# Optimization experiments

Hardware: AMD Instinct MI355X
Metric: run time of the kernel (lower is better)

## Reference

```python
import jax, jax.numpy as jnp
import numpy as np

B, K, D = 8192, 8192, 512

def setup_inputs() -> dict:
    key = jax.random.key(0)
    k1, k2 = jax.random.split(key)
    z_e = jax.random.normal(k1, (B, D), dtype=jnp.float32)
    # codebook: kaiming-uniform-initialized parameter; random normal scaled similarly is fine for a numeric baseline
    codebook = jax.random.normal(k2, (K, D), dtype=jnp.float32)
    return {"z_e": z_e, "codebook": codebook}

def reference(z_e, codebook):
    # Euclidean distances via dot-product expansion (same math as
    # torch.norm(z_e[:,None]-codebook[None], dim=-1) without the [B,K,D] intermediate):
    # d^2 = ||z||^2 - 2 z.c + ||c||^2
    z_sq = jnp.sum(z_e * z_e, axis=-1, keepdims=True)          # [B,1]
    c_sq = jnp.sum(codebook * codebook, axis=-1)               # [K]
    cross = jnp.einsum('bd,kd->bk', z_e, codebook)             # [B,K] GEMM
    d2 = jnp.maximum(z_sq - 2.0 * cross + c_sq[None, :], 0.0)  # clamp fp negatives
    distances = jnp.sqrt(d2)                                   # [B,K]
    indices = jnp.argmin(distances, axis=-1)                   # [B]
    z_q = jnp.take(codebook, indices, axis=0)                  # [B,D] gather
    return (z_q, indices)
```

## Files before the change

kernel.cpp:

```cpp
#include <hip/hip_runtime.h>


constexpr int Bn = 8192;
constexpr int Kn = 8192;
constexpr int Dn = 512;

using half8  = __attribute__((ext_vector_type(8)))  _Float16;
using f32x16 = __attribute__((ext_vector_type(16))) float;

#define WS_CSQ  0u
#define WS_ZSQ  (32u*1024u)
#define WS_MAX  (64u*1024u)
#define WS_CNT  (64u*1024u + 64u)
#define WS_WL   (96u*1024u)
#define WS_PART (1u*1024u*1024u)
#define WS_P2   WS_PART
#define WS_CIMG (10u*1024u*1024u)
#define WS_ZIMG (19u*1024u*1024u)

typedef __attribute__((address_space(3))) void       as3_void;
typedef const __attribute__((address_space(1))) void as1_cvoid;

#define MFMA16 __builtin_amdgcn_mfma_f32_32x32x16_f16


__global__ __launch_bounds__(256) void prep_kernel(const float* __restrict__ Z,
                                                   const float* __restrict__ Cb,
                                                   char* __restrict__ ws) {
  const int w = threadIdx.x >> 6, lane = threadIdx.x & 63;
  const int rid = blockIdx.x * 4 + w;
  if (blockIdx.x == 0 && threadIdx.x == 0) *(int*)(ws + WS_CNT) = 0;
  const bool isZ = rid < Bn;
  const int r = isZ ? rid : rid - Bn;
  const float* src = (isZ ? Z : Cb) + (size_t)r * Dn + lane * 8;
  const float4 v0 = *reinterpret_cast<const float4*>(src);
  const float4 v1 = *reinterpret_cast<const float4*>(src + 4);
  const float f[8] = {v0.x, v0.y, v0.z, v0.w, v1.x, v1.y, v1.z, v1.w};
  float ss = 0.f;
  _Float16 h[8];
#pragma unroll
  for (int j = 0; j < 8; ++j) { ss += f[j] * f[j]; h[j] = (_Float16)f[j]; }
#pragma unroll
  for (int off = 32; off; off >>= 1) ss += __shfl_xor(ss, off);
  const half8 vh = {h[0], h[1], h[2], h[3], h[4], h[5], h[6], h[7]};
  const int kt = lane >> 1, kh = lane & 1;
  int grp, rr, tbase, fr;
  char* img;
  if (isZ) {
    grp = (r >> 5) & 7; rr = r & 31; tbase = (r >> 8) * 33; fr = 512;
    img = ws + WS_ZIMG;
  } else {
    grp = (r >> 5) & 3; rr = r & 31; tbase = (r >> 7) * 33; fr = 256;
    img = ws + WS_CIMG;
  }
  const size_t chunk = (size_t)(tbase + kt) * fr + grp * 64 + kh * 32 + rr;
  *reinterpret_cast<half8*>(img + chunk * 16) = vh;
  if (lane < 2) {
    half8 ev = {0, 0, 0, 0, 0, 0, 0, 0};
    if (lane == 0) {
      if (isZ) { ev[0] = (_Float16)1.f; ev[1] = (_Float16)1.f; }
      else {
        const _Float16 hi = (_Float16)(-0.5f * ss);
        ev[0] = hi; ev[1] = (_Float16)(-0.5f * ss - (float)hi);
      }
    }
    const size_t ec = (size_t)(tbase + 32) * fr + grp * 64 + lane * 32 + rr;
    *reinterpret_cast<half8*>(img + ec * 16) = ev;
  }
  if (lane == 0) {
    if (isZ) ((float*)(ws + WS_ZSQ))[r] = ss;
    else {
      ((float*)(ws + WS_CSQ))[r] = ss;
      atomicMax((int*)(ws + WS_MAX), __float_as_int(ss));
    }
  }
}

__global__ __launch_bounds__(256, 2) void vq_pass1(char* __restrict__ ws) {
  __shared__ uint4 lds4[1536];
  char* lds = (char*)lds4;
  const int t = threadIdx.x, lane = t & 63, w = t >> 6;
  const int wm = w >> 1, wn = w & 1;
  const int zblk = blockIdx.x >> 4, split = blockIdx.x & 15;
  const int r31 = lane & 31, kh = lane >> 5;
  const char* CI = ws + WS_CIMG;
  const char* ZI = ws + WS_ZIMG;
  const size_t l16 = (size_t)lane * 16;
  const size_t zsrc = (size_t)zblk * 33 * 8192 + (size_t)w * 2048 + l16;
  const size_t abase = (size_t)(wm * 2) * 1024 + l16;

  float qs1[4], qs2[4];
  int qi1[4];
#pragma unroll
  for (int nb = 0; nb < 4; ++nb) { qs1[nb] = -3e38f; qs2[nb] = -3e38f; qi1[nb] = 0x7fffffff; }

  f32x16 acc[2][4] = {};
  half8 aA0, aA1, aB0, aB1;

  auto STAGE = [&](int kv, int bsel) {
    const char* s = ZI + zsrc + (size_t)kv * 8192;
    char* d = lds + bsel * 8192 + w * 2048;
    __builtin_amdgcn_global_load_lds((as1_cvoid*)(s), (as3_void*)(d), 16, 0, 0);
    __builtin_amdgcn_global_load_lds((as1_cvoid*)(s + 1024), (as3_void*)(d + 1024), 16, 0, 0);
  };

  STAGE(0, 0);
  STAGE(1, 1);
  {
    const char* s = CI + (size_t)(split * 4 * 33 + 0) * 4096 + abase;
    aA0 = *reinterpret_cast<const half8*>(s);
    aA1 = *reinterpret_cast<const half8*>(s + 1024);
  }
  asm volatile("s_waitcnt vmcnt(0)" ::: "memory");
  __builtin_amdgcn_s_barrier();

  int kt = 0, panel = 0, cur = 0, stg = 2;
#pragma unroll 2
  for (int u = 0; u < 132; ++u) {
    int k1 = kt + 1, p1 = panel;
    if (k1 == 33) { k1 = 0; ++p1; }
    int k2 = kt + 2, p2v = panel;
    if (k2 >= 33) { k2 -= 33; ++p2v; }
    if (u + 1 < 132) {
      const char* s = CI + (size_t)((split * 4 + p1) * 33 + k1) * 4096 + abase;
      if ((u & 1) == 0) {
        aB0 = *reinterpret_cast<const half8*>(s);
        aB1 = *reinterpret_cast<const half8*>(s + 1024);
      } else {
        aA0 = *reinterpret_cast<const half8*>(s);
        aA1 = *reinterpret_cast<const half8*>(s + 1024);
      }
    }
    if (u + 2 < 132) STAGE(k2, stg);
    const char* bb = lds + cur * 8192 + (size_t)wn * 4096 + l16;
    const half8 b0 = *reinterpret_cast<const half8*>(bb);
    const half8 b1 = *reinterpret_cast<const half8*>(bb + 1024);
    const half8 b2 = *reinterpret_cast<const half8*>(bb + 2048);
    const half8 b3 = *reinterpret_cast<const half8*>(bb + 3072);
    const half8 a0 = (u & 1) ? aB0 : aA0;
    const half8 a1 = (u & 1) ? aB1 : aA1;
    acc[0][0] = MFMA16(a0, b0, acc[0][0], 0, 0, 0);
    acc[0][1] = MFMA16(a0, b1, acc[0][1], 0, 0, 0);
    acc[0][2] = MFMA16(a0, b2, acc[0][2], 0, 0, 0);
    acc[0][3] = MFMA16(a0, b3, acc[0][3], 0, 0, 0);
    acc[1][0] = MFMA16(a1, b0, acc[1][0], 0, 0, 0);
    acc[1][1] = MFMA16(a1, b1, acc[1][1], 0, 0, 0);
    acc[1][2] = MFMA16(a1, b2, acc[1][2], 0, 0, 0);
    acc[1][3] = MFMA16(a1, b3, acc[1][3], 0, 0, 0);
    if (kt == 32) {
      const int cbase = split * 512 + panel * 128 + wm * 64 + 4 * kh;
#pragma unroll
      for (int nb = 0; nb < 4; ++nb) {
        float m1 = qs1[nb], m2 = qs2[nb];
        int i1 = qi1[nb];
#pragma unroll
        for (int ms = 0; ms < 2; ++ms)
#pragma unroll
          for (int r = 0; r < 16; ++r) {
            const float a = acc[ms][nb][r];
            const int ci = cbase + ms * 32 + (r & 3) + 8 * (r >> 2);
            const bool gt = (a > m1) || (a == m1 && ci < i1);
            const float nm2 = gt ? m1 : fmaxf(m2, a);
            m1 = gt ? a : m1;
            i1 = gt ? ci : i1;
            m2 = nm2;
          }
        qs1[nb] = m1; qs2[nb] = m2; qi1[nb] = i1;
      }
#pragma unroll
      for (int ms = 0; ms < 2; ++ms)
#pragma unroll
        for (int nb = 0; nb < 4; ++nb) acc[ms][nb] = (f32x16)0.f;
    }
    if (u < 130) asm volatile("s_waitcnt vmcnt(4)" ::: "memory");
    else         asm volatile("s_waitcnt vmcnt(2)" ::: "memory");
    __builtin_amdgcn_s_barrier();
    ++kt;
    if (kt == 33) { kt = 0; ++panel; }
    cur = (cur == 2) ? 0 : cur + 1;
    stg = (stg == 2) ? 0 : stg + 1;
  }

  float4* part = (float4*)(ws + WS_PART);
  const int bucket = split * 4 + wm * 2 + kh;
#pragma unroll
  for (int nb = 0; nb < 4; ++nb) {
    const int row = zblk * 256 + wn * 128 + nb * 32 + r31;
    part[(size_t)row * 64 + bucket] =
        make_float4(-2.f * qs1[nb], (float)qi1[nb], -2.f * qs2[nb], 0.f);
  }
}

__global__ __launch_bounds__(64) void gather_finalize(const float* __restrict__ Z,
                                                      const float* __restrict__ Cb,
                                                      char* __restrict__ ws,
                                                      float* __restrict__ zq,
                                                      float* __restrict__ idx_out) {
  const int row = blockIdx.x, l = threadIdx.x;
  const float4 q = ((const float4*)(ws + WS_PART))[(size_t)row * 64 + l];
  float s1 = q.x;
  int i1 = (int)q.y;
#pragma unroll
  for (int off = 1; off <= 32; off <<= 1) {
    const float os = __shfl_xor(s1, off); const int oi = __shfl_xor(i1, off);
    if (os < s1 || (os == s1 && oi < i1)) { s1 = os; i1 = oi; }
  }
  const float zs = ((const float*)(ws + WS_ZSQ))[row];
  const float cmax = __int_as_float(*(const int*)(ws + WS_MAX));
  const float thr = s1 + 4.0e-3f * sqrtf(zs * cmax) + 0.05f;
  int cnt = (q.x <= thr ? 1 : 0) + (q.z <= thr ? 1 : 0);
  int hide = (q.z <= thr) ? 1 : 0;
#pragma unroll
  for (int off = 1; off <= 32; off <<= 1) {
    cnt += __shfl_xor(cnt, off);
    hide |= __shfl_xor(hide, off);
  }
  if (cnt >= 5 || hide) {
    if (l == 0) {
      const int pos = atomicAdd((int*)(ws + WS_CNT), 1);
      if (pos < Bn) ((int*)(ws + WS_WL))[pos] = row;
    }
    return;
  }
  const float* csq = (const float*)(ws + WS_CSQ);
  const float4 z0 = *reinterpret_cast<const float4*>(Z + (size_t)row * Dn + l * 8);
  const float4 z1 = *reinterpret_cast<const float4*>(Z + (size_t)row * Dn + l * 8 + 4);
  float mycand = (q.x <= thr) ? q.x : 3e38f;
  const int myid = (int)q.y;
  float best_s = 3e38f;
  int best_i = 0x7fffffff;
  for (int it = 0; it < 4; ++it) {
    float cs_ = mycand;
    int ci_ = myid;
#pragma unroll
    for (int off = 1; off <= 32; off <<= 1) {
      const float os = __shfl_xor(cs_, off); const int oi = __shfl_xor(ci_, off);
      if (os < cs_ || (os == cs_ && oi < ci_)) { cs_ = os; ci_ = oi; }
    }
    if (cs_ > thr) break;
    if (myid == ci_) mycand = 3e38f;
    const float4 c0 = *reinterpret_cast<const float4*>(Cb + (size_t)ci_ * Dn + l * 8);
    const float4 c1 = *reinterpret_cast<const float4*>(Cb + (size_t)ci_ * Dn + l * 8 + 4);
    float pa = z0.x * c0.x + z0.y * c0.y + z0.z * c0.z + z0.w * c0.w +
               z1.x * c1.x + z1.y * c1.y + z1.z * c1.z + z1.w * c1.w;
#pragma unroll
    for (int off = 1; off <= 32; off <<= 1) pa += __shfl_xor(pa, off);
    const float se = csq[ci_] - 2.f * pa;
    if (se < best_s || (se == best_s && ci_ < best_i)) { best_s = se; best_i = ci_; }
  }
  const float4 o0 = *reinterpret_cast<const float4*>(Cb + (size_t)best_i * Dn + l * 8);
  const float4 o1 = *reinterpret_cast<const float4*>(Cb + (size_t)best_i * Dn + l * 8 + 4);
  *reinterpret_cast<float4*>(zq + (size_t)row * Dn + l * 8) = o0;
  *reinterpret_cast<float4*>(zq + (size_t)row * Dn + l * 8 + 4) = o1;
  if (l == 0) idx_out[row] = (float)best_i;
}

__global__ __launch_bounds__(256) void rescue1(const float* __restrict__ Z,
                                               const float* __restrict__ Cb,
                                               char* __restrict__ ws) {
  const int cntRaw = *(const int*)(ws + WS_CNT);
  const int cnt = cntRaw > Bn ? Bn : cntRaw;
  if (cnt == 0) return;
  const int tiles_r = (cnt + 63) >> 6;
  const int total = tiles_r * 128;
  const int* wl = (const int*)(ws + WS_WL);
  const float* csq = (const float*)(ws + WS_CSQ);
  float2* p2 = (float2*)(ws + WS_P2);
  __shared__ float As[32][68];
  __shared__ float Bs[32][68];
  __shared__ int wlrows[64];
  const int t = threadIdx.x;
  const int tx = t & 15, ty = t >> 4;
  const int sr = t >> 3, sc = (t & 7) * 4;
  for (int tile = blockIdx.x; tile < total; tile += gridDim.x) {
    const int tr = tile >> 7, tc = tile & 127;
    __syncthreads();
    if (t < 64) {
      const int wi = tr * 64 + t;
      wlrows[t] = wl[wi < cnt ? wi : cnt - 1];
    }
    __syncthreads();
    float acc[4][4] = {};
    for (int k0 = 0; k0 < Dn; k0 += 32) {
#pragma unroll
      for (int rr = 0; rr < 2; ++rr) {
        const int m = sr + rr * 32;
        const float4 v = *reinterpret_cast<const float4*>(Z + (size_t)wlrows[m] * Dn + k0 + sc);
        As[sc + 0][m] = v.x; As[sc + 1][m] = v.y; As[sc + 2][m] = v.z; As[sc + 3][m] = v.w;
        const float4 u = *reinterpret_cast<const float4*>(Cb + (size_t)(tc * 64 + m) * Dn + k0 + sc);
        Bs[sc + 0][m] = u.x; Bs[sc + 1][m] = u.y; Bs[sc + 2][m] = u.z; Bs[sc + 3][m] = u.w;
      }
      __syncthreads();
#pragma unroll
      for (int k = 0; k < 32; ++k) {
        const float4 a = *reinterpret_cast<const float4*>(&As[k][ty * 4]);
        const float4 b = *reinterpret_cast<const float4*>(&Bs[k][tx * 4]);
        acc[0][0] += a.x * b.x; acc[0][1] += a.x * b.y; acc[0][2] += a.x * b.z; acc[0][3] += a.x * b.w;
        acc[1][0] += a.y * b.x; acc[1][1] += a.y * b.y; acc[1][2] += a.y * b.z; acc[1][3] += a.y * b.w;
        acc[2][0] += a.z * b.x; acc[2][1] += a.z * b.y; acc[2][2] += a.z * b.z; acc[2][3] += a.z * b.w;
        acc[3][0] += a.w * b.x; acc[3][1] += a.w * b.y; acc[3][2] += a.w * b.z; acc[3][3] += a.w * b.w;
      }
      __syncthreads();
    }
#pragma unroll
    for (int i = 0; i < 4; ++i) {
      float bsv = 3e38f;
      int bi = 0;
#pragma unroll
      for (int j = 0; j < 4; ++j) {
        const int n = tc * 64 + tx * 4 + j;
        const float s = csq[n] - 2.f * acc[i][j];
        if (s < bsv || (s == bsv && n < bi)) { bsv = s; bi = n; }
      }
#pragma unroll
      for (int off = 1; off <= 8; off <<= 1) {
        const float os = __shfl_xor(bsv, off); const int oi = __shfl_xor(bi, off);
        if (os < bsv || (os == bsv && oi < bi)) { bsv = os; bi = oi; }
      }
      if (tx == 0) p2[(size_t)(tr * 64 + ty * 4 + i) * 128 + tc] = make_float2(bsv, (float)bi);
    }
  }
}

__global__ __launch_bounds__(64) void rescue2(const float* __restrict__ Cb,
                                              char* __restrict__ ws,
                                              float* __restrict__ zq,
                                              float* __restrict__ idx_out) {
  const int cntRaw = *(const int*)(ws + WS_CNT);
  const int cnt = cntRaw > Bn ? Bn : cntRaw;
  const int* wl = (const int*)(ws + WS_WL);
  const float2* p2 = (const float2*)(ws + WS_P2);
  const int l = threadIdx.x;
  for (int rr = blockIdx.x; rr < cnt; rr += gridDim.x) {
    const int row = wl[rr];
    const float2 e1 = p2[(size_t)rr * 128 + l];
    const float2 e2 = p2[(size_t)rr * 128 + 64 + l];
    float bs_ = e1.x;
    int bi_ = (int)e1.y;
    if (e2.x < bs_ || (e2.x == bs_ && (int)e2.y < bi_)) { bs_ = e2.x; bi_ = (int)e2.y; }
#pragma unroll
    for (int off = 1; off <= 32; off <<= 1) {
      const float os = __shfl_xor(bs_, off); const int oi = __shfl_xor(bi_, off);
      if (os < bs_ || (os == bs_ && oi < bi_)) { bs_ = os; bi_ = oi; }
    }
    const float4 c0 = *reinterpret_cast<const float4*>(Cb + (size_t)bi_ * Dn + l * 8);
    const float4 c1 = *reinterpret_cast<const float4*>(Cb + (size_t)bi_ * Dn + l * 8 + 4);
    *reinterpret_cast<float4*>(zq + (size_t)row * Dn + l * 8) = c0;
    *reinterpret_cast<float4*>(zq + (size_t)row * Dn + l * 8 + 4) = c1;
    if (l == 0) idx_out[row] = (float)bi_;
  }
}

extern "C" void kernel_launch(void* const* d_in, const int* in_sizes, int n_in,
                              void* d_out, int out_size, void* d_ws, size_t ws_size,
                              hipStream_t stream) {
  const float* Z = (const float*)d_in[0];
  const float* C = (const float*)d_in[1];
  float* out = (float*)d_out;
  char* ws = (char*)d_ws;

  prep_kernel<<<4096, 256, 0, stream>>>(Z, C, ws);
  vq_pass1<<<512, 256, 0, stream>>>(ws);
  gather_finalize<<<Bn, 64, 0, stream>>>(Z, C, ws, out, out + (size_t)Bn * Dn);
  rescue1<<<512, 256, 0, stream>>>(Z, C, ws);
  rescue2<<<256, 64, 0, stream>>>(C, ws, out, out + (size_t)Bn * Dn);
}
```

Baseline: 266.1 us.

## Split prep into sums and coalesced image kernels, tighten rescue threshold, skip unambiguous refinement

Prep is split into a squared-norm kernel and a separate fp16 image builder that writes whole 16-element chunks with coalesced stores. The fp16 margin threshold drops from 4e-3 to 2.1e-3, so fewer rows go to exact refinement or the rescue path. Rows with a single candidate skip the fp32 re-check. The finalize kernel packs four rows per block, and the split mapping is permuted for L2 locality. The tighter threshold raises the risk of picking a wrong argmin, and the extra launch and doubled LDS declaration (possibly unused) add cost.

```diff
diff --git a/kernel.cpp b/kernel.cpp
--- a/kernel.cpp
+++ b/kernel.cpp
@@ -13,10 +13,10 @@
 #define WS_MAX  (64u*1024u)
 #define WS_CNT  (64u*1024u + 64u)
 #define WS_WL   (96u*1024u)
-#define WS_PART (1u*1024u*1024u)
-#define WS_P2   WS_PART
-#define WS_CIMG (10u*1024u*1024u)
-#define WS_ZIMG (19u*1024u*1024u)
+#define WS_P1   (1u*1024u*1024u)
+#define WS_P2R  WS_P1
+#define WS_CIMG (13u*1024u*1024u)
+#define WS_ZIMG (22u*1024u*1024u)
 
 typedef __attribute__((address_space(3))) void       as3_void;
 typedef const __attribute__((address_space(1))) void as1_cvoid;
@@ -24,9 +24,9 @@
 #define MFMA16 __builtin_amdgcn_mfma_f32_32x32x16_f16
 
 
-__global__ __launch_bounds__(256) void prep_kernel(const float* __restrict__ Z,
-                                                   const float* __restrict__ Cb,
-                                                   char* __restrict__ ws) {
+__global__ __launch_bounds__(256) void prep_sums(const float* __restrict__ Z,
+                                                 const float* __restrict__ Cb,
+                                                 char* __restrict__ ws) {
   const int w = threadIdx.x >> 6, lane = threadIdx.x & 63;
   const int rid = blockIdx.x * 4 + w;
   if (blockIdx.x == 0 && threadIdx.x == 0) *(int*)(ws + WS_CNT) = 0;
@@ -35,38 +35,10 @@
   const float* src = (isZ ? Z : Cb) + (size_t)r * Dn + lane * 8;
   const float4 v0 = *reinterpret_cast<const float4*>(src);
   const float4 v1 = *reinterpret_cast<const float4*>(src + 4);
-  const float f[8] = {v0.x, v0.y, v0.z, v0.w, v1.x, v1.y, v1.z, v1.w};
-  float ss = 0.f;
-  _Float16 h[8];
-#pragma unroll
-  for (int j = 0; j < 8; ++j) { ss += f[j] * f[j]; h[j] = (_Float16)f[j]; }
+  float ss = v0.x * v0.x + v0.y * v0.y + v0.z * v0.z + v0.w * v0.w +
+             v1.x * v1.x + v1.y * v1.y + v1.z * v1.z + v1.w * v1.w;
 #pragma unroll
   for (int off = 32; off; off >>= 1) ss += __shfl_xor(ss, off);
-  const half8 vh = {h[0], h[1], h[2], h[3], h[4], h[5], h[6], h[7]};
-  const int kt = lane >> 1, kh = lane & 1;
-  int grp, rr, tbase, fr;
-  char* img;
-  if (isZ) {
-    grp = (r >> 5) & 7; rr = r & 31; tbase = (r >> 8) * 33; fr = 512;
-    img = ws + WS_ZIMG;
-  } else {
-    grp = (r >> 5) & 3; rr = r & 31; tbase = (r >> 7) * 33; fr = 256;
-    img = ws + WS_CIMG;
-  }
-  const size_t chunk = (size_t)(tbase + kt) * fr + grp * 64 + kh * 32 + rr;
-  *reinterpret_cast<half8*>(img + chunk * 16) = vh;
-  if (lane < 2) {
-    half8 ev = {0, 0, 0, 0, 0, 0, 0, 0};
-    if (lane == 0) {
-      if (isZ) { ev[0] = (_Float16)1.f; ev[1] = (_Float16)1.f; }
-      else {
-        const _Float16 hi = (_Float16)(-0.5f * ss);
-        ev[0] = hi; ev[1] = (_Float16)(-0.5f * ss - (float)hi);
-      }
-    }
-    const size_t ec = (size_t)(tbase + 32) * fr + grp * 64 + lane * 32 + rr;
-    *reinterpret_cast<half8*>(img + ec * 16) = ev;
-  }
   if (lane == 0) {
     if (isZ) ((float*)(ws + WS_ZSQ))[r] = ss;
     else {
@@ -76,12 +48,73 @@
   }
 }
 
+__global__ __launch_bounds__(256) void prep_img(const float* __restrict__ Z,
+                                                const float* __restrict__ Cb,
+                                                char* __restrict__ ws) {
+  const int w = threadIdx.x >> 6, lane = threadIdx.x & 63;
+  const int wid = blockIdx.x * 4 + w;
+  char* CI = ws + WS_CIMG;
+  char* ZI = ws + WS_ZIMG;
+  if (wid < 2048) {
+    const bool isC = wid < 1024;
+    const int f = isC ? wid : wid - 1024;
+    const int koct = f & 3;
+    const int grp = isC ? ((f >> 2) & 3) : ((f >> 2) & 7);
+    const int blk = isC ? (f >> 4) : (f >> 5);
+    const int rowbase = (isC ? blk * 128 : blk * 256) + grp * 32;
+    const float* src = isC ? Cb : Z;
+    char* img = isC ? CI : ZI;
+    const int fr = isC ? 256 : 512;
+    const int ktsel = lane & 1, rr = lane >> 1;
+    const float* rowp = src + (size_t)(rowbase + rr) * Dn;
+#pragma unroll
+    for (int kp = 0; kp < 4; ++kp) {
+      const int kt = koct * 8 + kp * 2 + ktsel;
+      const float4 v0 = *reinterpret_cast<const float4*>(rowp + kt * 16);
+      const float4 v1 = *reinterpret_cast<const float4*>(rowp + kt * 16 + 4);
+      const float4 v2 = *reinterpret_cast<const float4*>(rowp + kt * 16 + 8);
+      const float4 v3 = *reinterpret_cast<const float4*>(rowp + kt * 16 + 12);
+      const float fl[16] = {v0.x, v0.y, v0.z, v0.w, v1.x, v1.y, v1.z, v1.w,
+                            v2.x, v2.y, v2.z, v2.w, v3.x, v3.y, v3.z, v3.w};
+      _Float16 h[16];
+#pragma unroll
+      for (int j = 0; j < 16; ++j) h[j] = (_Float16)fl[j];
+      const half8 lo8 = {h[0], h[1], h[2], h[3], h[4], h[5], h[6], h[7]};
+      const half8 hi8 = {h[8], h[9], h[10], h[11], h[12], h[13], h[14], h[15]};
+      char* fb = img + ((size_t)(blk * 33 + kt) * fr + grp * 64) * 16;
+      *reinterpret_cast<half8*>(fb + rr * 16) = lo8;
+      *reinterpret_cast<half8*>(fb + 512 + rr * 16) = hi8;
+    }
+  } else if (wid < 2304) {
+    const int e = wid - 2048;
+    const int grp = e & 3, blk = e >> 2;
+    half8 ev = {};
+    if (lane < 32) {
+      const float ss = ((const float*)(ws + WS_CSQ))[blk * 128 + grp * 32 + lane];
+      const _Float16 hi = (_Float16)(-0.5f * ss);
+      ev[0] = hi;
+      ev[1] = (_Float16)(-0.5f * ss - (float)hi);
+    }
+    char* fb = CI + ((size_t)(blk * 33 + 32) * 256 + grp * 64) * 16;
+    *reinterpret_cast<half8*>(fb + lane * 16) = ev;
+  } else {
+    const int e = wid - 2304;
+    const int grp = e & 7, blk = e >> 3;
+    half8 ev = {};
+    if (lane < 32) { ev[0] = (_Float16)1.f; ev[1] = (_Float16)1.f; }
+    char* fb = ZI + ((size_t)(blk * 33 + 32) * 512 + grp * 64) * 16;
+    *reinterpret_cast<half8*>(fb + lane * 16) = ev;
+  }
+}
+
 __global__ __launch_bounds__(256, 2) void vq_pass1(char* __restrict__ ws) {
-  __shared__ uint4 lds4[1536];
+  __shared__ uint4 lds4[3072];
   char* lds = (char*)lds4;
   const int t = threadIdx.x, lane = t & 63, w = t >> 6;
   const int wm = w >> 1, wn = w & 1;
-  const int zblk = blockIdx.x >> 4, split = blockIdx.x & 15;
+  const int bid = blockIdx.x;
+  const int zblk = bid >> 4;
+  const int split = ((bid & 7) << 1) | ((bid >> 3) & 1);
   const int r31 = lane & 31, kh = lane >> 5;
   const char* CI = ws + WS_CIMG;
   const char* ZI = ws + WS_ZIMG;
@@ -119,8 +152,8 @@
   for (int u = 0; u < 132; ++u) {
     int k1 = kt + 1, p1 = panel;
     if (k1 == 33) { k1 = 0; ++p1; }
-    int k2 = kt + 2, p2v = panel;
-    if (k2 >= 33) { k2 -= 33; ++p2v; }
+    int k2 = kt + 2;
+    if (k2 >= 33) k2 -= 33;
     if (u + 1 < 132) {
       const char* s = CI + (size_t)((split * 4 + p1) * 33 + k1) * 4096 + abase;
       if ((u & 1) == 0) {
@@ -181,7 +214,7 @@
     stg = (stg == 2) ? 0 : stg + 1;
   }
 
-  float4* part = (float4*)(ws + WS_PART);
+  float4* part = (float4*)(ws + WS_P1);
   const int bucket = split * 4 + wm * 2 + kh;
 #pragma unroll
   for (int nb = 0; nb < 4; ++nb) {
@@ -191,13 +224,14 @@
   }
 }
 
-__global__ __launch_bounds__(64) void gather_finalize(const float* __restrict__ Z,
-                                                      const float* __restrict__ Cb,
-                                                      char* __restrict__ ws,
-                                                      float* __restrict__ zq,
-                                                      float* __restrict__ idx_out) {
-  const int row = blockIdx.x, l = threadIdx.x;
-  const float4 q = ((const float4*)(ws + WS_PART))[(size_t)row * 64 + l];
+__global__ __launch_bounds__(256) void gather_finalize(const float* __restrict__ Z,
+                                                       const float* __restrict__ Cb,
+                                                       char* __restrict__ ws,
+                                                       float* __restrict__ zq,
+                                                       float* __restrict__ idx_out) {
+  const int w = threadIdx.x >> 6, l = threadIdx.x & 63;
+  const int row = blockIdx.x * 4 + w;
+  const float4 q = ((const float4*)(ws + WS_P1))[(size_t)row * 64 + l];
   float s1 = q.x;
   int i1 = (int)q.y;
 #pragma unroll
@@ -207,7 +241,7 @@
   }
   const float zs = ((const float*)(ws + WS_ZSQ))[row];
   const float cmax = __int_as_float(*(const int*)(ws + WS_MAX));
-  const float thr = s1 + 4.0e-3f * sqrtf(zs * cmax) + 0.05f;
+  const float thr = s1 + 2.1e-3f * sqrtf(zs * cmax) + 0.05f;
   int cnt = (q.x <= thr ? 1 : 0) + (q.z <= thr ? 1 : 0);
   int hide = (q.z <= thr) ? 1 : 0;
 #pragma unroll
@@ -222,37 +256,41 @@
     }
     return;
   }
-  const float* csq = (const float*)(ws + WS_CSQ);
-  const float4 z0 = *reinterpret_cast<const float4*>(Z + (size_t)row * Dn + l * 8);
-  const float4 z1 = *reinterpret_cast<const float4*>(Z + (size_t)row * Dn + l * 8 + 4);
-  float mycand = (q.x <= thr) ? q.x : 3e38f;
-  const int myid = (int)q.y;
-  float best_s = 3e38f;
-  int best_i = 0x7fffffff;
-  for (int it = 0; it < 4; ++it) {
-    float cs_ = mycand;
-    int ci_ = myid;
-#pragma unroll
-    for (int off = 1; off <= 32; off <<= 1) {
-      const float os = __shfl_xor(cs_, off); const int oi = __shfl_xor(ci_, off);
-      if (os < cs_ || (os == cs_ && oi < ci_)) { cs_ = os; ci_ = oi; }
-    }
-    if (cs_ > thr) break;
-    if (myid == ci_) mycand = 3e38f;
-    const float4 c0 = *reinterpret_cast<const float4*>(Cb + (size_t)ci_ * Dn + l * 8);
-    const float4 c1 = *reinterpret_cast<const float4*>(Cb + (size_t)ci_ * Dn + l * 8 + 4);
-    float pa = z0.x * c0.x + z0.y * c0.y + z0.z * c0.z + z0.w * c0.w +
-               z1.x * c1.x + z1.y * c1.y + z1.z * c1.z + z1.w * c1.w;
-#pragma unroll
-    for (int off = 1; off <= 32; off <<= 1) pa += __shfl_xor(pa, off);
-    const float se = csq[ci_] - 2.f * pa;
-    if (se < best_s || (se == best_s && ci_ < best_i)) { best_s = se; best_i = ci_; }
-  }
-  const float4 o0 = *reinterpret_cast<const float4*>(Cb + (size_t)best_i * Dn + l * 8);
-  const float4 o1 = *reinterpret_cast<const float4*>(Cb + (size_t)best_i * Dn + l * 8 + 4);
+  int winner = i1;
+  if (cnt > 1) {
+    const float* csq = (const float*)(ws + WS_CSQ);
+    const float4 z0 = *reinterpret_cast<const float4*>(Z + (size_t)row * Dn + l * 8);
+    const float4 z1 = *reinterpret_cast<const float4*>(Z + (size_t)row * Dn + l * 8 + 4);
+    float mycand = (q.x <= thr) ? q.x : 3e38f;
+    const int myid = (int)q.y;
+    float best_s = 3e38f;
+    int best_i = 0x7fffffff;
+    for (int it = 0; it < 4; ++it) {
+      float cs_ = mycand;
+      int ci_ = myid;
+#pragma unroll
+      for (int off = 1; off <= 32; off <<= 1) {
+        const float os = __shfl_xor(cs_, off); const int oi = __shfl_xor(ci_, off);
+        if (os < cs_ || (os == cs_ && oi < ci_)) { cs_ = os; ci_ = oi; }
+      }
+      if (cs_ > thr) break;
+      if (myid == ci_) mycand = 3e38f;
+      const float4 c0 = *reinterpret_cast<const float4*>(Cb + (size_t)ci_ * Dn + l * 8);
+      const float4 c1 = *reinterpret_cast<const float4*>(Cb + (size_t)ci_ * Dn + l * 8 + 4);
+      float pa = z0.x * c0.x + z0.y * c0.y + z0.z * c0.z + z0.w * c0.w +
+                 z1.x * c1.x + z1.y * c1.y + z1.z * c1.z + z1.w * c1.w;
+#pragma unroll
+      for (int off = 1; off <= 32; off <<= 1) pa += __shfl_xor(pa, off);
+      const float se = csq[ci_] - 2.f * pa;
+      if (se < best_s || (se == best_s && ci_ < best_i)) { best_s = se; best_i = ci_; }
+    }
+    winner = best_i;
+  }
+  const float4 o0 = *reinterpret_cast<const float4*>(Cb + (size_t)winner * Dn + l * 8);
+  const float4 o1 = *reinterpret_cast<const float4*>(Cb + (size_t)winner * Dn + l * 8 + 4);
   *reinterpret_cast<float4*>(zq + (size_t)row * Dn + l * 8) = o0;
   *reinterpret_cast<float4*>(zq + (size_t)row * Dn + l * 8 + 4) = o1;
-  if (l == 0) idx_out[row] = (float)best_i;
+  if (l == 0) idx_out[row] = (float)winner;
 }
 
 __global__ __launch_bounds__(256) void rescue1(const float* __restrict__ Z,
@@ -265,7 +303,7 @@
   const int total = tiles_r * 128;
   const int* wl = (const int*)(ws + WS_WL);
   const float* csq = (const float*)(ws + WS_CSQ);
-  float2* p2 = (float2*)(ws + WS_P2);
+  float2* p2 = (float2*)(ws + WS_P2R);
   __shared__ float As[32][68];
   __shared__ float Bs[32][68];
   __shared__ int wlrows[64];
@@ -329,7 +367,7 @@
   const int cntRaw = *(const int*)(ws + WS_CNT);
   const int cnt = cntRaw > Bn ? Bn : cntRaw;
   const int* wl = (const int*)(ws + WS_WL);
-  const float2* p2 = (const float2*)(ws + WS_P2);
+  const float2* p2 = (const float2*)(ws + WS_P2R);
   const int l = threadIdx.x;
   for (int rr = blockIdx.x; rr < cnt; rr += gridDim.x) {
     const int row = wl[rr];
@@ -359,9 +397,10 @@
   float* out = (float*)d_out;
   char* ws = (char*)d_ws;
 
-  prep_kernel<<<4096, 256, 0, stream>>>(Z, C, ws);
+  prep_sums<<<4096, 256, 0, stream>>>(Z, C, ws);
+  prep_img<<<640, 256, 0, stream>>>(Z, C, ws);
   vq_pass1<<<512, 256, 0, stream>>>(ws);
-  gather_finalize<<<Bn, 64, 0, stream>>>(Z, C, ws, out, out + (size_t)Bn * Dn);
+  gather_finalize<<<2048, 256, 0, stream>>>(Z, C, ws, out, out + (size_t)Bn * Dn);
   rescue1<<<512, 256, 0, stream>>>(Z, C, ws);
   rescue2<<<256, 64, 0, stream>>>(C, ws, out, out + (size_t)Bn * Dn);
 }
```

Result: no change. 268.2 us (+0.8%).
